# Kernel tuning notes

Measured on AMD Instinct MI355X. Metric: run time of the kernel, lower is better.

Reference implementation:

```python
import jax, jax.numpy as jnp
import numpy as np

N = 4096
INP_DIM = 256
EMB_DIM = 256
ALPHA = 0.01  # LeakyReLU negative slope
NEG_INF = -9.0e15


def _xavier(key, shape, gain=1.414):
    fan_in, fan_out = shape[0], shape[1]
    limit = gain * np.sqrt(6.0 / (fan_in + fan_out))
    return jax.random.uniform(key, shape, jnp.float32, -limit, limit)


def setup_inputs() -> dict:
    key = jax.random.key(0)
    ks = jax.random.split(key, 9)
    inp = {
        "input": jax.random.normal(ks[0], (N, INP_DIM), jnp.float32),
        "adj": jax.random.randint(ks[1], (N, N), 0, 2, jnp.int32),
        "W0": _xavier(ks[2], (INP_DIM, EMB_DIM)),
        "W1": _xavier(ks[3], (EMB_DIM, EMB_DIM)),
        "a1": _xavier(ks[4], (2 * EMB_DIM, 1)),
        "W2": _xavier(ks[5], (EMB_DIM, EMB_DIM)),
        "a2": _xavier(ks[6], (2 * EMB_DIM, 1)),
        "W3": _xavier(ks[7], (EMB_DIM, EMB_DIM)),
        "a3": _xavier(ks[8], (2 * EMB_DIM, 1)),
    }
    return inp


def _gat_layer(h, adj, W, a):
    # h: [N, F_in], W: [F_in, F], a: [2F, 1]
    Wh = h @ W                       # [N, F]
    F_out = Wh.shape[1]
    # e_ij = leakyrelu([Wh_i || Wh_j] @ a) = leakyrelu(Wh_i@a1 + Wh_j@a2)
    f1 = Wh @ a[:F_out]              # [N, 1]
    f2 = Wh @ a[F_out:]              # [N, 1]
    e = jax.nn.leaky_relu(f1 + f2.T, ALPHA)            # [N, N]
    att = jnp.where(adj > 0, e, NEG_INF)
    att = jax.nn.softmax(att, axis=1)                    # masked softmax over neighbors
    h_prime = att @ Wh                                   # [N, F]
    return jax.nn.elu(h_prime)                           # concat=True -> ELU


def reference(input, adj, W0, W1, a1, W2, a2, W3, a3):
    h = input @ W0                   # GAT-level projection
    h = _gat_layer(h, adj, W1, a1)
    h = _gat_layer(h, adj, W2, a2)
    h = _gat_layer(h, adj, W3, a3)
    return h
```

## Files before the change

kernel.cpp:

```cpp
#include <hip/hip_runtime.h>
#include <hip/hip_bf16.h>
#include <hip/hip_fp16.h>
#include <cstdint>
#include <cstddef>

#define NN 4096
#define FD 256
#define WPR 64

typedef __attribute__((ext_vector_type(8))) unsigned short ushort8v;
typedef __attribute__((ext_vector_type(4))) unsigned short ushort4v;
typedef __attribute__((ext_vector_type(8))) short short8;
typedef __attribute__((ext_vector_type(4))) float float4v;

#define C1 30.0f
#define C2 0.3f

static __device__ __forceinline__ unsigned short f2bf(float x) {
    union { float f; unsigned int u; } v; v.f = x;
    unsigned int r = v.u + 0x7FFFu + ((v.u >> 16) & 1u);
    return (unsigned short)(r >> 16);
}

static __device__ __forceinline__ short8 as_s8(ushort8v v) {
    union { ushort8v u; short8 s; } x; x.u = v; return x.s;
}

__global__ __launch_bounds__(256) void setup(const int* __restrict__ adj,
                                             const float* __restrict__ input,
                                             const float* __restrict__ W0, const float* __restrict__ W1,
                                             const float* __restrict__ W2, const float* __restrict__ W3,
                                             unsigned long long* __restrict__ bits,
                                             unsigned short* __restrict__ hb,
                                             unsigned short* __restrict__ Wbt,
                                             float* __restrict__ f1f2) {
    const int b = blockIdx.x;
    const int t = threadIdx.x;
    if (b < 4096) {
        const int wave = t >> 6, lane = t & 63;
        const int* arow = adj + (size_t)b * NN;
        #pragma unroll
        for (int it = 0; it < NN / 256; ++it) {
            int j = it * 256 + wave * 64 + lane;
            unsigned long long m = __ballot(arow[j] > 0);
            if (lane == 0) bits[(size_t)b * WPR + (it * 4 + wave)] = m;
        }
        hb[(size_t)b * 256 + t] = f2bf(input[(size_t)b * 256 + t]);
    } else if (b < 5120) {
        int idx = (b - 4096) * 256 + t;
        int mat = idx >> 16;
        int within = idx & 65535;
        int n = within >> 8, k = within & 255;
        const float* W = (mat == 0) ? W0 : (mat == 1) ? W1 : (mat == 2) ? W2 : W3;
        Wbt[idx] = f2bf(W[k * 256 + n]);
    } else {
        #pragma unroll
        for (int i = 0; i < 24; ++i) {
            int pos = i * 1024 + (b - 5120) * 256 + t;
            f1f2[pos] = 0.f;
        }
    }
}

__global__ __launch_bounds__(256) void proj_gemm(const unsigned short* __restrict__ A,
                                                 const unsigned short* __restrict__ Bt,
                                                 const float* __restrict__ av,
                                                 float* __restrict__ f1f2,
                                                 unsigned short* __restrict__ Cbt,
                                                 unsigned short* __restrict__ Crow) {
    const int t = threadIdx.x;
    const int bm = blockIdx.x >> 2, bn = blockIdx.x & 3;
    const int m0 = bm * 32, n0 = bn * 64;
    __shared__ unsigned short As[32 * 264];
    __shared__ unsigned short Bs[64 * 264];
    const int lane = t & 63, wave = t >> 6;
    const int wm = (wave >> 1) * 16, wn = (wave & 1) * 32;
    const int g = lane >> 4, ml = lane & 15;
    {
        int ar = t >> 3, ac0 = (t & 7) * 8;
        #pragma unroll
        for (int i = 0; i < 4; ++i) {
            int col = ac0 + i * 64;
            *(ushort8v*)&As[ar * 264 + col] = *(const ushort8v*)&A[(size_t)(m0 + ar) * 256 + col];
        }
        int br = t >> 2, bc0 = (t & 3) * 8;
        #pragma unroll
        for (int i = 0; i < 8; ++i) {
            int col = bc0 + i * 32;
            *(ushort8v*)&Bs[br * 264 + col] = *(const ushort8v*)&Bt[(size_t)(n0 + br) * 256 + col];
        }
    }
    __syncthreads();
    float4v acc[2] = {{0.f,0.f,0.f,0.f},{0.f,0.f,0.f,0.f}};
    #pragma unroll
    for (int kk = 0; kk < 256; kk += 32) {
        const int kc = kk + g * 8;
        short8 a = as_s8(*(const ushort8v*)&As[(wm + ml) * 264 + kc]);
        #pragma unroll
        for (int fn = 0; fn < 2; ++fn) {
            short8 b = as_s8(*(const ushort8v*)&Bs[(wn + fn * 16 + ml) * 264 + kc]);
            acc[fn] = __builtin_amdgcn_mfma_f32_16x16x32_bf16(a, b, acc[fn], 0, 0, 0);
        }
    }

    const int rb = wm + g * 4;
    if (Crow) {
        #pragma unroll
        for (int fn = 0; fn < 2; ++fn)
            #pragma unroll
            for (int r = 0; r < 4; ++r)
                Crow[(size_t)(m0 + rb + r) * 256 + n0 + wn + fn * 16 + ml] = f2bf(acc[fn][r]);
    }

    if (f1f2) {
        float a1c[2], a2c[2];
        #pragma unroll
        for (int fn = 0; fn < 2; ++fn) {
            a1c[fn] = av[n0 + wn + fn * 16 + ml];
            a2c[fn] = av[256 + n0 + wn + fn * 16 + ml];
        }
        #pragma unroll
        for (int r = 0; r < 4; ++r) {
            float s1 = acc[0][r] * a1c[0] + acc[1][r] * a1c[1];
            float s2 = acc[0][r] * a2c[0] + acc[1][r] * a2c[1];
            #pragma unroll
            for (int off = 1; off < 16; off <<= 1) {
                s1 += __shfl_xor(s1, off, 64);
                s2 += __shfl_xor(s2, off, 64);
            }
            if (ml == 0) {
                int row = m0 + rb + r;
                atomicAdd(&f1f2[row], s1);
                atomicAdd(&f1f2[4096 + row], s2);
            }
        }
    }

    if (Cbt) {
        unsigned short* T = As;
        __syncthreads();
        #pragma unroll
        for (int fn = 0; fn < 2; ++fn)
            #pragma unroll
            for (int r = 0; r < 4; ++r)
                T[(wn + fn * 16 + ml) * 40 + rb + r] = f2bf(acc[fn][r]);
        __syncthreads();
        const int tr = t >> 2, tc = (t & 3) * 8;
        *(ushort8v*)&Cbt[(size_t)(n0 + tr) * 4096 + m0 + tc] = *(const ushort8v*)&T[tr * 40 + tc];
    }
}

__global__ __launch_bounds__(256) void rowcoef(const unsigned long long* __restrict__ bits,
                                               const float* __restrict__ f1f2,
                                               float4* __restrict__ rowco,
                                               float2* __restrict__ tab2g) {
    __shared__ float2 tl[4096];
    const int t = threadIdx.x;
    const float* f2p = f1f2 + 4096;
    #pragma unroll
    for (int i = 0; i < 16; ++i) {
        float v = f2p[i * 256 + t];
        float2 pr = make_float2(__expf(v - C1), __expf(0.01f * v - C2));
        tl[i * 256 + t] = pr;
        if (blockIdx.x == 0) tab2g[i * 256 + t] = pr;
    }
    __syncthreads();
    const int lane = t & 63, wave = t >> 6;
    for (int rr = 0; rr < 2; ++rr) {
        const int row = blockIdx.x * 8 + wave * 2 + rr;
        const unsigned long long wl = bits[(size_t)row * WPR + lane];
        const float f1r = f1f2[row];
        const float th = __expf(-f1r - C1);
        float mx = 0.f, S1 = 0.f, S2 = 0.f;
        #pragma unroll 16
        for (int b = 0; b < 64; ++b) {
            unsigned long long w = __shfl(wl, b, 64);
            bool bit = (w >> lane) & 1ULL;
            float2 v = tl[b * 64 + lane];
            float ebm = bit ? v.x : 0.f;
            mx = fmaxf(mx, ebm);
            bool cond = v.x > th;
            S1 += (bit && cond)  ? v.x : 0.f;
            S2 += (bit && !cond) ? v.y : 0.f;
        }
        #pragma unroll
        for (int off = 1; off < 64; off <<= 1) {
            mx = fmaxf(mx, __shfl_xor(mx, off, 64));
            S1 += __shfl_xor(S1, off, 64);
            S2 += __shfl_xor(S2, off, 64);
        }
        if (lane == 0) {
            float M  = C1 + __logf(mx);
            float fm_ = f1r + M;
            float m  = fm_ > 0.f ? fm_ : 0.01f * fm_;
            float alpha = __expf(fminf(f1r + C1 - m, 60.f));
            float gamma = __expf(fminf(0.01f * (f1r + C1) - m, 60.f));
            float inv = 1.0f / (alpha * S1 + gamma * S2);
            rowco[row] = make_float4(alpha * inv, gamma * inv, th, 0.f);
        }
    }
}

__global__ __launch_bounds__(256, 4) void att_gemm(const unsigned long long* __restrict__ bits,
                                                   const float4* __restrict__ rowco,
                                                   const float* __restrict__ tab2f,
                                                   const unsigned short* __restrict__ Bt,
                                                   unsigned short* __restrict__ parth, int kchunk) {
    const int t = threadIdx.x;
    const int bm = blockIdx.x & 31;
    const int bn = (blockIdx.x >> 5) & 1;
    const int ks = blockIdx.x >> 6;
    const int m0 = bm * 128, n0 = bn * 128;
    const int k0 = ks * kchunk;
    __shared__ unsigned short Bs[2][128 * 40];
    const int lane = t & 63, wave = t >> 6;
    const int g = lane >> 4, ml = lane & 15;

    const int srow = t >> 1, skh = (t & 1) * 16;
    const unsigned short* bsrc = Bt + (size_t)(n0 + srow) * 4096 + skh;

    float pA[2], pG[2], th[2];
    const unsigned long long* brow[2];
    #pragma unroll
    for (int fm = 0; fm < 2; ++fm) {
        int row = m0 + wave * 32 + fm * 16 + ml;
        float4 rc = rowco[row];
        pA[fm] = rc.x; pG[fm] = rc.y; th[fm] = rc.z;
        brow[fm] = bits + (size_t)row * WPR;
    }

    float4v acc[2][8];
    #pragma unroll
    for (int i = 0; i < 2; ++i)
        #pragma unroll
        for (int j = 0; j < 8; ++j) acc[i][j] = (float4v){0.f, 0.f, 0.f, 0.f};

    {
        ushort8v b0 = *(const ushort8v*)&bsrc[k0];
        ushort8v b1 = *(const ushort8v*)&bsrc[k0 + 8];
        *(ushort8v*)&Bs[0][srow * 40 + skh]     = b0;
        *(ushort8v*)&Bs[0][srow * 40 + skh + 8] = b1;
    }
    __syncthreads();

    const int nsteps = kchunk >> 5;
    for (int i = 0; i < nsteps; ++i) {
        const int kk = k0 + i * 32;
        const int p = i & 1;
        ushort8v nb0, nb1;
        if (i + 1 < nsteps) {
            nb0 = *(const ushort8v*)&bsrc[kk + 32];
            nb1 = *(const ushort8v*)&bsrc[kk + 40];
        }
        const int word = kk >> 6;
        const int kb = (kk & 63) + g * 8;
        unsigned long long wv0 = brow[0][word];
        unsigned long long wv1 = brow[1][word];
        const float4v* q = (const float4v*)&tab2f[2 * (kk + g * 8)];
        float4v q0 = q[0], q1 = q[1], q2 = q[2], q3 = q[3];
        short8 afr[2];
        #pragma unroll
        for (int fm = 0; fm < 2; ++fm) {
            unsigned int wh = (unsigned int)((fm ? wv1 : wv0) >> kb);
            ushort8v af;
            #pragma unroll
            for (int jj = 0; jj < 4; ++jj) {
                float4v v = (jj == 0) ? q0 : (jj == 1) ? q1 : (jj == 2) ? q2 : q3;
                float x0 = ((wh >> (2 * jj)) & 1u)     ? (v[0] > th[fm] ? pA[fm] * v[0] : pG[fm] * v[1]) : 0.f;
                float x1 = ((wh >> (2 * jj + 1)) & 1u) ? (v[2] > th[fm] ? pA[fm] * v[2] : pG[fm] * v[3]) : 0.f;
                union { __hip_bfloat162 b2; unsigned int u; } cv;
                cv.b2 = __float22bfloat162_rn(make_float2(x0, x1));
                ((unsigned int*)&af)[jj] = cv.u;
            }
            afr[fm] = as_s8(af);
        }
        #pragma unroll
        for (int fn = 0; fn < 8; ++fn) {
            short8 b = as_s8(*(const ushort8v*)&Bs[p][(fn * 16 + ml) * 40 + g * 8]);
            acc[0][fn] = __builtin_amdgcn_mfma_f32_16x16x32_bf16(afr[0], b, acc[0][fn], 0, 0, 0);
            acc[1][fn] = __builtin_amdgcn_mfma_f32_16x16x32_bf16(afr[1], b, acc[1][fn], 0, 0, 0);
        }
        if (i + 1 < nsteps) {
            *(ushort8v*)&Bs[1 - p][srow * 40 + skh]     = nb0;
            *(ushort8v*)&Bs[1 - p][srow * 40 + skh + 8] = nb1;
            __syncthreads();
        }
    }

    unsigned short* pbase = parth + ((size_t)ks << 20) + (size_t)(bm * 2 + bn) * 16384;
    #pragma unroll
    for (int fm = 0; fm < 2; ++fm)
        #pragma unroll
        for (int fn = 0; fn < 8; ++fn) {
            ushort4v v4;
            #pragma unroll
            for (int r = 0; r < 4; ++r) {
                __half h = __float2half(acc[fm][fn][r]);
                v4[r] = *(unsigned short*)&h;
            }
            *(ushort4v*)&pbase[((wave * 16 + fm * 8 + fn) * 64 + lane) * 4] = v4;
        }
}

template<int NS>
__global__ __launch_bounds__(256) void att_reduce(const unsigned short* __restrict__ parth,
                                                  float* __restrict__ outf,
                                                  unsigned short* __restrict__ hrow) {
    const int flat = (blockIdx.x * 256 + threadIdx.x) * 8;
    float s[8] = {0.f, 0.f, 0.f, 0.f, 0.f, 0.f, 0.f, 0.f};
    #pragma unroll
    for (int sp = 0; sp < NS; ++sp) {
        ushort8v v = *(const ushort8v*)&parth[((size_t)sp << 20) + flat];
        #pragma unroll
        for (int j = 0; j < 8; ++j) {
            unsigned short u = v[j];
            s[j] += __half2float(*(__half*)&u);
        }
    }
    const int tile  = flat >> 14;
    const int inner = flat & 16383;
    const int widx = inner >> 8;
    const int ls   = (inner >> 2) & 63;
    const int bm = tile >> 1, bn = tile & 1;
    const int wavea = widx >> 4, fm = (widx >> 3) & 1, fn = widx & 7;
    const int g = ls >> 4, ml = ls & 15;
    const int row0 = bm * 128 + wavea * 32 + fm * 16 + g * 4;
    const int col  = bn * 128 + fn * 16 + ml;
    #pragma unroll
    for (int r = 0; r < 4; ++r) {
        float x0 = s[r];
        float x1 = s[4 + r];
        x0 = x0 > 0.f ? x0 : (__expf(x0) - 1.f);
        x1 = x1 > 0.f ? x1 : (__expf(x1) - 1.f);
        unsigned int hp = (unsigned int)f2bf(x0) | ((unsigned int)f2bf(x1) << 16);
        *(unsigned int*)&hrow[(size_t)(row0 + r) * 256 + col] = hp;
        if (outf) *(float2*)&outf[(size_t)(row0 + r) * 256 + col] = make_float2(x0, x1);
    }
}

static void launch_reduce(int SPLIT, const unsigned short* parth, float* outf,
                          unsigned short* hrow, hipStream_t stream) {
    switch (SPLIT) {
        case 16: att_reduce<16><<<512, 256, 0, stream>>>(parth, outf, hrow); break;
        case 8:  att_reduce<8><<<512, 256, 0, stream>>>(parth, outf, hrow); break;
        case 4:  att_reduce<4><<<512, 256, 0, stream>>>(parth, outf, hrow); break;
        case 2:  att_reduce<2><<<512, 256, 0, stream>>>(parth, outf, hrow); break;
        default: att_reduce<1><<<512, 256, 0, stream>>>(parth, outf, hrow); break;
    }
}

extern "C" void kernel_launch(void* const* d_in, const int* in_sizes, int n_in,
                              void* d_out, int out_size, void* d_ws, size_t ws_size,
                              hipStream_t stream) {
    const float* input = (const float*)d_in[0];
    const int*   adj   = (const int*)d_in[1];
    const float* W0    = (const float*)d_in[2];
    const float* W1    = (const float*)d_in[3];
    const float* a1    = (const float*)d_in[4];
    const float* W2    = (const float*)d_in[5];
    const float* a2    = (const float*)d_in[6];
    const float* W3    = (const float*)d_in[7];
    const float* a3    = (const float*)d_in[8];
    float* out = (float*)d_out;
    char* ws = (char*)d_ws;

    unsigned long long* bits = (unsigned long long*)(ws);
    unsigned short* h0   = (unsigned short*)(ws + (2u << 20));
    unsigned short* h1   = (unsigned short*)(ws + (4u << 20));
    unsigned short* Whbt = (unsigned short*)(ws + (6u << 20));
    unsigned short* Wbt  = (unsigned short*)(ws + (8u << 20));
    float*  f1f2  = (float*)(ws + (9u << 20));
    float4* rowco = (float4*)(ws + (10u << 20));
    float2* tab2  = (float2*)(ws + (10u << 20) + (256u << 10));
    unsigned short* parth = (unsigned short*)(ws + (13u << 20));

    const size_t base = 13u << 20;
    int SPLIT = 16;
    while (SPLIT > 1 && base + (size_t)SPLIT * (2u << 20) > ws_size) SPLIT >>= 1;
    const int kchunk = NN / SPLIT;

    float* f1f2_l[3] = { f1f2, f1f2 + 8192, f1f2 + 16384 };

    setup<<<5124, 256, 0, stream>>>(adj, input, W0, W1, W2, W3, bits, h0, Wbt, f1f2);

    proj_gemm<<<512, 256, 0, stream>>>(h0, Wbt + 0 * 65536, nullptr, nullptr, nullptr, h1);

    proj_gemm<<<512, 256, 0, stream>>>(h1, Wbt + 1 * 65536, a1, f1f2_l[0], Whbt, nullptr);
    rowcoef<<<512, 256, 0, stream>>>(bits, f1f2_l[0], rowco, tab2);
    att_gemm<<<64 * SPLIT, 256, 0, stream>>>(bits, rowco, (const float*)tab2, Whbt, parth, kchunk);
    launch_reduce(SPLIT, parth, nullptr, h0, stream);

    proj_gemm<<<512, 256, 0, stream>>>(h0, Wbt + 2 * 65536, a2, f1f2_l[1], Whbt, nullptr);
    rowcoef<<<512, 256, 0, stream>>>(bits, f1f2_l[1], rowco, tab2);
    att_gemm<<<64 * SPLIT, 256, 0, stream>>>(bits, rowco, (const float*)tab2, Whbt, parth, kchunk);
    launch_reduce(SPLIT, parth, nullptr, h1, stream);

    proj_gemm<<<512, 256, 0, stream>>>(h1, Wbt + 3 * 65536, a3, f1f2_l[2], Whbt, nullptr);
    rowcoef<<<512, 256, 0, stream>>>(bits, f1f2_l[2], rowco, tab2);
    att_gemm<<<64 * SPLIT, 256, 0, stream>>>(bits, rowco, (const float*)tab2, Whbt, parth, kchunk);
    launch_reduce(SPLIT, parth, out, h0, stream);
}
```

Measured before the change: 282.1 us.

## Template att_gemm on step count, prefetch adjacency words and table, use fmax select

The attention GEMM is templated on a compile-time step count so its main loop fully unrolls. All adjacency bit-words a block needs are loaded into registers up front, and the exp-table vectors for the next k-step are prefetched alongside the B tile. The per-element branch on the threshold becomes an fmaxf of the two scaled candidates, which assumes that max gives the same result as the threshold select. Launch bounds drop from 4 to 3 blocks per CU to make room for the extra registers, and the split factor is limited to 16 or 8.

```diff
diff --git a/kernel.cpp b/kernel.cpp
--- a/kernel.cpp
+++ b/kernel.cpp
@@ -201,32 +201,34 @@
     }
 }
 
-__global__ __launch_bounds__(256, 4) void att_gemm(const unsigned long long* __restrict__ bits,
+template<int NSTEPS>
+__global__ __launch_bounds__(256, 3) void att_gemm(const unsigned long long* __restrict__ bits,
                                                    const float4* __restrict__ rowco,
                                                    const float* __restrict__ tab2f,
                                                    const unsigned short* __restrict__ Bt,
-                                                   unsigned short* __restrict__ parth, int kchunk) {
+                                                   unsigned short* __restrict__ parth) {
     const int t = threadIdx.x;
     const int bm = blockIdx.x & 31;
     const int bn = (blockIdx.x >> 5) & 1;
     const int ks = blockIdx.x >> 6;
     const int m0 = bm * 128, n0 = bn * 128;
-    const int k0 = ks * kchunk;
+    const int k0 = ks * (NSTEPS * 32);
     __shared__ unsigned short Bs[2][128 * 40];
     const int lane = t & 63, wave = t >> 6;
     const int g = lane >> 4, ml = lane & 15;
-
     const int srow = t >> 1, skh = (t & 1) * 16;
     const unsigned short* bsrc = Bt + (size_t)(n0 + srow) * 4096 + skh;
 
-    float pA[2], pG[2], th[2];
-    const unsigned long long* brow[2];
+    float pA[2], pG[2];
+    unsigned long long wpre[2][NSTEPS / 2];
     #pragma unroll
     for (int fm = 0; fm < 2; ++fm) {
         int row = m0 + wave * 32 + fm * 16 + ml;
         float4 rc = rowco[row];
-        pA[fm] = rc.x; pG[fm] = rc.y; th[fm] = rc.z;
-        brow[fm] = bits + (size_t)row * WPR;
+        pA[fm] = rc.x; pG[fm] = rc.y;
+        const unsigned long long* brow = bits + (size_t)row * WPR + (k0 >> 6);
+        #pragma unroll
+        for (int w = 0; w < NSTEPS / 2; ++w) wpre[fm][w] = brow[w];
     }
 
     float4v acc[2][8];
@@ -235,39 +237,42 @@
         #pragma unroll
         for (int j = 0; j < 8; ++j) acc[i][j] = (float4v){0.f, 0.f, 0.f, 0.f};
 
+    float4v tq0, tq1, tq2, tq3;
     {
         ushort8v b0 = *(const ushort8v*)&bsrc[k0];
         ushort8v b1 = *(const ushort8v*)&bsrc[k0 + 8];
+        const float4v* q = (const float4v*)&tab2f[2 * (k0 + g * 8)];
+        tq0 = q[0]; tq1 = q[1]; tq2 = q[2]; tq3 = q[3];
         *(ushort8v*)&Bs[0][srow * 40 + skh]     = b0;
         *(ushort8v*)&Bs[0][srow * 40 + skh + 8] = b1;
     }
     __syncthreads();
 
-    const int nsteps = kchunk >> 5;
-    for (int i = 0; i < nsteps; ++i) {
+    #pragma unroll
+    for (int i = 0; i < NSTEPS; ++i) {
         const int kk = k0 + i * 32;
         const int p = i & 1;
         ushort8v nb0, nb1;
-        if (i + 1 < nsteps) {
+        float4v nt0, nt1, nt2, nt3;
+        if (i + 1 < NSTEPS) {
             nb0 = *(const ushort8v*)&bsrc[kk + 32];
             nb1 = *(const ushort8v*)&bsrc[kk + 40];
-        }
-        const int word = kk >> 6;
-        const int kb = (kk & 63) + g * 8;
-        unsigned long long wv0 = brow[0][word];
-        unsigned long long wv1 = brow[1][word];
-        const float4v* q = (const float4v*)&tab2f[2 * (kk + g * 8)];
-        float4v q0 = q[0], q1 = q[1], q2 = q[2], q3 = q[3];
+            const float4v* q = (const float4v*)&tab2f[2 * (kk + 32 + g * 8)];
+            nt0 = q[0]; nt1 = q[1]; nt2 = q[2]; nt3 = q[3];
+        }
+        const int sh = (i & 1) * 32 + g * 8;
         short8 afr[2];
         #pragma unroll
         for (int fm = 0; fm < 2; ++fm) {
-            unsigned int wh = (unsigned int)((fm ? wv1 : wv0) >> kb);
+            unsigned int wh = (unsigned int)(wpre[fm][i >> 1] >> sh);
             ushort8v af;
             #pragma unroll
             for (int jj = 0; jj < 4; ++jj) {
-                float4v v = (jj == 0) ? q0 : (jj == 1) ? q1 : (jj == 2) ? q2 : q3;
-                float x0 = ((wh >> (2 * jj)) & 1u)     ? (v[0] > th[fm] ? pA[fm] * v[0] : pG[fm] * v[1]) : 0.f;
-                float x1 = ((wh >> (2 * jj + 1)) & 1u) ? (v[2] > th[fm] ? pA[fm] * v[2] : pG[fm] * v[3]) : 0.f;
+                float4v v = (jj == 0) ? tq0 : (jj == 1) ? tq1 : (jj == 2) ? tq2 : tq3;
+                float x0 = fmaxf(pA[fm] * v[0], pG[fm] * v[1]);
+                float x1 = fmaxf(pA[fm] * v[2], pG[fm] * v[3]);
+                x0 = ((wh >> (2 * jj)) & 1u)     ? x0 : 0.f;
+                x1 = ((wh >> (2 * jj + 1)) & 1u) ? x1 : 0.f;
                 union { __hip_bfloat162 b2; unsigned int u; } cv;
                 cv.b2 = __float22bfloat162_rn(make_float2(x0, x1));
                 ((unsigned int*)&af)[jj] = cv.u;
@@ -280,10 +285,11 @@
             acc[0][fn] = __builtin_amdgcn_mfma_f32_16x16x32_bf16(afr[0], b, acc[0][fn], 0, 0, 0);
             acc[1][fn] = __builtin_amdgcn_mfma_f32_16x16x32_bf16(afr[1], b, acc[1][fn], 0, 0, 0);
         }
-        if (i + 1 < nsteps) {
+        if (i + 1 < NSTEPS) {
             *(ushort8v*)&Bs[1 - p][srow * 40 + skh]     = nb0;
             *(ushort8v*)&Bs[1 - p][srow * 40 + skh + 8] = nb1;
             __syncthreads();
+            tq0 = nt0; tq1 = nt1; tq2 = nt2; tq3 = nt3;
         }
     }
 
@@ -338,15 +344,17 @@
     }
 }
 
+static void launch_att(int SPLIT, const unsigned long long* bits, const float4* rowco,
+                       const float* tab2f, const unsigned short* Bt,
+                       unsigned short* parth, hipStream_t stream) {
+    if (SPLIT == 16) att_gemm<8><<<64 * 16, 256, 0, stream>>>(bits, rowco, tab2f, Bt, parth);
+    else             att_gemm<16><<<64 * 8, 256, 0, stream>>>(bits, rowco, tab2f, Bt, parth);
+}
+
 static void launch_reduce(int SPLIT, const unsigned short* parth, float* outf,
                           unsigned short* hrow, hipStream_t stream) {
-    switch (SPLIT) {
-        case 16: att_reduce<16><<<512, 256, 0, stream>>>(parth, outf, hrow); break;
-        case 8:  att_reduce<8><<<512, 256, 0, stream>>>(parth, outf, hrow); break;
-        case 4:  att_reduce<4><<<512, 256, 0, stream>>>(parth, outf, hrow); break;
-        case 2:  att_reduce<2><<<512, 256, 0, stream>>>(parth, outf, hrow); break;
-        default: att_reduce<1><<<512, 256, 0, stream>>>(parth, outf, hrow); break;
-    }
+    if (SPLIT == 16) att_reduce<16><<<512, 256, 0, stream>>>(parth, outf, hrow);
+    else             att_reduce<8><<<512, 256, 0, stream>>>(parth, outf, hrow);
 }
 
 extern "C" void kernel_launch(void* const* d_in, const int* in_sizes, int n_in,
@@ -375,9 +383,7 @@
     unsigned short* parth = (unsigned short*)(ws + (13u << 20));
 
     const size_t base = 13u << 20;
-    int SPLIT = 16;
-    while (SPLIT > 1 && base + (size_t)SPLIT * (2u << 20) > ws_size) SPLIT >>= 1;
-    const int kchunk = NN / SPLIT;
+    int SPLIT = (base + 16u * (2u << 20) <= ws_size) ? 16 : 8;
 
     float* f1f2_l[3] = { f1f2, f1f2 + 8192, f1f2 + 16384 };
 
@@ -387,16 +393,16 @@
 
     proj_gemm<<<512, 256, 0, stream>>>(h1, Wbt + 1 * 65536, a1, f1f2_l[0], Whbt, nullptr);
     rowcoef<<<512, 256, 0, stream>>>(bits, f1f2_l[0], rowco, tab2);
-    att_gemm<<<64 * SPLIT, 256, 0, stream>>>(bits, rowco, (const float*)tab2, Whbt, parth, kchunk);
+    launch_att(SPLIT, bits, rowco, (const float*)tab2, Whbt, parth, stream);
     launch_reduce(SPLIT, parth, nullptr, h0, stream);
 
     proj_gemm<<<512, 256, 0, stream>>>(h0, Wbt + 2 * 65536, a2, f1f2_l[1], Whbt, nullptr);
     rowcoef<<<512, 256, 0, stream>>>(bits, f1f2_l[1], rowco, tab2);
-    att_gemm<<<64 * SPLIT, 256, 0, stream>>>(bits, rowco, (const float*)tab2, Whbt, parth, kchunk);
+    launch_att(SPLIT, bits, rowco, (const float*)tab2, Whbt, parth, stream);
     launch_reduce(SPLIT, parth, nullptr, h1, stream);
 
     proj_gemm<<<512, 256, 0, stream>>>(h1, Wbt + 3 * 65536, a3, f1f2_l[2], Whbt, nullptr);
     rowcoef<<<512, 256, 0, stream>>>(bits, f1f2_l[2], rowco, tab2);
-    att_gemm<<<64 * SPLIT, 256, 0, stream>>>(bits, rowco, (const float*)tab2, Whbt, parth, kchunk);
+    launch_att(SPLIT, bits, rowco, (const float*)tab2, Whbt, parth, stream);
     launch_reduce(SPLIT, parth, out, h0, stream);
 }
```

Measured after the change: 277.0 us. Within noise of the previous version (-1.8%).
